# Performance work log

Hardware: AMD Instinct MI355X
Metric: run time of the kernel (lower is better)

Reference implementation:

```python
import jax, jax.numpy as jnp
import numpy as np

TOKENS, D_IN, D_OUT = 8192, 4096, 4096

def setup_inputs() -> dict:
    key = jax.random.key(0)
    k1, k2, k3 = jax.random.split(key, 3)
    x = jax.random.normal(k1, (TOKENS, D_IN), dtype=jnp.float32)
    # original init: uniform(-1, 1) on weights of shape [out, in]
    w_pos = jax.random.uniform(k2, (D_OUT, D_IN), dtype=jnp.float32, minval=-1.0, maxval=1.0)
    w_neg = jax.random.uniform(k3, (D_OUT, D_IN), dtype=jnp.float32, minval=-1.0, maxval=1.0)
    return {"x": x, "w_pos": w_pos, "w_neg": w_neg}

def _ste_binarize(w):
    # (w > 0).float() in fwd, identity grad (STE): stop_grad(bin - w) + w
    b = (w > 0).astype(w.dtype)
    return jax.lax.stop_gradient(b - w) + w

def reference(x, w_pos, w_neg):
    tern_pos = _ste_binarize(w_pos)  # [O, I]
    tern_neg = _ste_binarize(w_neg)  # [O, I]
    # y = x @ tern_pos^T - x @ tern_neg^T  (biases unused in original forward)
    y = jnp.einsum('ti,oi->to', x, tern_pos) - jnp.einsum('ti,oi->to', x, tern_neg)
    return y
```

## Files before the change

kernel.cpp:

```cpp
#include <hip/hip_runtime.h>
#include <stdint.h>


#define TOKENS 8192
#define DIN    4096
#define DOUT   4096

typedef __bf16  bf16x8  __attribute__((ext_vector_type(8)));
typedef float   floatx4 __attribute__((ext_vector_type(4)));

__device__ __forceinline__ void async_copy16(const void* g, void* l) {
  __builtin_amdgcn_global_load_lds(
      (const __attribute__((address_space(1))) void*)g,
      (__attribute__((address_space(3))) void*)l, 16, 0, 0);
}

__device__ __forceinline__ unsigned short f2bf_rne(float f) {
  union { float f; uint32_t u; } v; v.f = f;
  uint32_t u = v.u;
  u += 0x7fffu + ((u >> 16) & 1u);
  return (unsigned short)(u >> 16);
}

__device__ __forceinline__ unsigned short tern_bits(float p, float n) {
  bool bp = p > 0.0f, bn = n > 0.0f;
  return (unsigned short)(bp == bn ? 0u : (bp ? 0x3f80u : 0xbf80u));
}

__global__ __launch_bounds__(256) void prep_kernel(
    const float4* __restrict__ x, ushort4* __restrict__ xb,
    const float4* __restrict__ wp, const float4* __restrict__ wn,
    ushort4* __restrict__ t) {
  const uint32_t bid = blockIdx.x;
  if (bid < 8192u) {
    const uint32_t stride = 8192u * 256u;
    uint32_t i = bid * 256u + threadIdx.x;
#pragma unroll
    for (int it = 0; it < 4; ++it, i += stride) {
      float4 v = x[i];
      ushort4 o;
      o.x = f2bf_rne(v.x); o.y = f2bf_rne(v.y);
      o.z = f2bf_rne(v.z); o.w = f2bf_rne(v.w);
      xb[i] = o;
    }
  } else {
    const uint32_t stride = 4096u * 256u;
    uint32_t i = (bid - 8192u) * 256u + threadIdx.x;
#pragma unroll
    for (int it = 0; it < 4; ++it, i += stride) {
      float4 p = wp[i];
      float4 n = wn[i];
      ushort4 o;
      o.x = tern_bits(p.x, n.x);
      o.y = tern_bits(p.y, n.y);
      o.z = tern_bits(p.z, n.z);
      o.w = tern_bits(p.w, n.w);
      t[i] = o;
    }
  }
}


#define LDS_BUF   65536u
#define LDS_B_OFF 32768u
#define LDS_KC    16384u

__global__ __launch_bounds__(512, 2) void gemm_bt(
    const unsigned short* __restrict__ A,
    const unsigned short* __restrict__ B,
    float* __restrict__ C)
{
  __shared__ __align__(16) char lds[131072];

  const int tid   = threadIdx.x;
  const int lane  = tid & 63;
  const int wid   = tid >> 6;
  const int waveM = wid >> 2;
  const int waveN = wid & 3;

  const uint32_t flat = blockIdx.x;
  const uint32_t swz  = ((flat & 7u) << 6) | (flat >> 3);
  const uint32_t bm = (swz >> 4) * 256u;
  const uint32_t bn = (swz & 15u) * 256u;

  const uint32_t srow  = (uint32_t)(tid >> 6) * 32u + (uint32_t)((tid & 63) >> 2);
  const uint32_t slot  = (uint32_t)(tid & 3);
  const uint32_t chnk  = slot ^ ((srow >> 1) & 3u);
  const uint32_t stA   = (bm + srow) * (DIN * 2u) + chnk * 16u;
  const uint32_t stB   = (bn + srow) * (DIN * 2u) + chnk * 16u;
  const uint32_t ldsSt = (uint32_t)(tid >> 6) * 2048u + (uint32_t)(tid & 63) * 16u;
  const char* Ab = (const char*)A;
  const char* Bb = (const char*)B;

  const int mrow = lane & 15;
  const int q    = lane >> 4;
  const int xs   = (q ^ ((mrow >> 1) & 3)) * 16;
  const uint32_t ldsBase =
      (uint32_t)(uintptr_t)(__attribute__((address_space(3))) char*)lds;
  const uint32_t aFragBase = (uint32_t)waveM * 8192u + (uint32_t)mrow * 64u + (uint32_t)xs;
  const uint32_t bFragBase = LDS_B_OFF + (uint32_t)waveN * 4096u
                           + (uint32_t)mrow * 64u + (uint32_t)xs;
  const uint32_t aA0 = ldsBase + aFragBase;
  const uint32_t aA1 = aA0 + LDS_BUF;
  const uint32_t bA0 = ldsBase + bFragBase;
  const uint32_t bA1 = bA0 + LDS_BUF;

  floatx4 acc[8][4];
#pragma unroll
  for (int m = 0; m < 8; ++m)
#pragma unroll
    for (int n = 0; n < 4; ++n)
      acc[m][n] = (floatx4)0.0f;

  floatx4 a0f[4], a1f[4], b0f[4], b1f[4];

#define DSR(DST, ADDR, IMM)                                                \
  asm volatile("ds_read_b128 %0, %1 offset:%c2"                            \
               : "=v"(DST) : "v"(ADDR), "i"(IMM))

#define IA4(DST, ADDR, KC, MH) do {                                        \
    DSR(DST[0], ADDR, (KC) * 16384 + ((MH) * 4 + 0) * 1024);               \
    DSR(DST[1], ADDR, (KC) * 16384 + ((MH) * 4 + 1) * 1024);               \
    DSR(DST[2], ADDR, (KC) * 16384 + ((MH) * 4 + 2) * 1024);               \
    DSR(DST[3], ADDR, (KC) * 16384 + ((MH) * 4 + 3) * 1024);               \
  } while (0)

#define IB2(DST, N0, ADDR, KC) do {                                        \
    DSR(DST[N0],     ADDR, (KC) * 16384 + ((N0)) * 1024);                  \
    DSR(DST[N0 + 1], ADDR, (KC) * 16384 + ((N0) + 1) * 1024);              \
  } while (0)

#define STAGE_A(BUF, KH, KB) do {                                          \
    uint32_t g_ = stA + (KB) + (KH) * 64u;                                 \
    uint32_t l_ = (BUF) * LDS_BUF + (KH) * LDS_KC + ldsSt;                 \
    async_copy16(Ab + g_,           lds + l_);                             \
    async_copy16(Ab + g_ + 131072u, lds + l_ + 1024u);                     \
  } while (0)

#define STAGE_B(BUF, KH, KB) do {                                          \
    uint32_t g_ = stB + (KB) + (KH) * 64u;                                 \
    uint32_t l_ = (BUF) * LDS_BUF + LDS_B_OFF + (KH) * LDS_KC + ldsSt;     \
    async_copy16(Bb + g_,           lds + l_);                             \
    async_copy16(Bb + g_ + 131072u, lds + l_ + 1024u);                     \
  } while (0)

#define PHASE(MH, AF, BF, ISSUE_STMT, STAGE_STMT) do {                     \
    asm volatile("s_waitcnt lgkmcnt(0)" ::: "memory");                     \
    asm volatile("s_waitcnt vmcnt(8)" ::: "memory");                       \
    __builtin_amdgcn_sched_barrier(0);                                     \
    ISSUE_STMT;                                                            \
    __builtin_amdgcn_sched_barrier(0);                                     \
    __builtin_amdgcn_s_setprio(1);                                         \
    _Pragma("unroll")                                                      \
    for (int m_ = 0; m_ < 4; ++m_)                                         \
      _Pragma("unroll")                                                    \
      for (int n_ = 0; n_ < 4; ++n_)                                       \
        acc[(MH) * 4 + m_][n_] = __builtin_amdgcn_mfma_f32_16x16x32_bf16(  \
            __builtin_bit_cast(bf16x8, AF[m_]),                            \
            __builtin_bit_cast(bf16x8, BF[n_]),                            \
            acc[(MH) * 4 + m_][n_], 0, 0, 0);                              \
    __builtin_amdgcn_s_setprio(0);                                         \
    STAGE_STMT;                                                            \
    __builtin_amdgcn_s_barrier();                                          \
  } while (0)

  STAGE_B(0, 0, 0u);
  STAGE_A(0, 0, 0u);
  STAGE_B(0, 1, 0u);
  STAGE_A(0, 1, 0u);
  STAGE_B(1, 0, 128u);
  STAGE_A(1, 0, 128u);
  STAGE_B(1, 1, 128u);
  asm volatile("s_waitcnt vmcnt(8)" ::: "memory");
  __builtin_amdgcn_s_barrier();
  IB2(b0f, 0, bA0, 0); IB2(b0f, 2, bA0, 0 + 0);
  DSR(b0f[0], bA0, 0); DSR(b0f[1], bA0, 1024);
  DSR(b0f[2], bA0, 2048); DSR(b0f[3], bA0, 3072);
  IA4(a0f, aA0, 0, 0);

#pragma unroll 1
  for (int i = 0; i < 32; ++i) {
    const uint32_t kb1 = (uint32_t)(2 * i + 1) * 128u;
    const uint32_t kb2 = (uint32_t)((2 * i + 2) & 63) * 128u;
    const uint32_t kb3 = (uint32_t)((2 * i + 3) & 63) * 128u;

    PHASE(0, a0f, b0f, { IA4(a1f, aA0, 0, 1); IB2(b1f, 0, bA0, 1); },
          STAGE_A(1, 1, kb1));
    PHASE(1, a1f, b0f, { IA4(a0f, aA0, 1, 0); IB2(b1f, 2, bA0, 1); },
          STAGE_B(0, 0, kb2));
    PHASE(0, a0f, b1f, { IA4(a1f, aA0, 1, 1); IB2(b0f, 0, bA1, 0); },
          STAGE_A(0, 0, kb2));
    PHASE(1, a1f, b1f, { IA4(a0f, aA1, 0, 0); IB2(b0f, 2, bA1, 0); },
          STAGE_B(0, 1, kb2));
    PHASE(0, a0f, b0f, { IA4(a1f, aA1, 0, 1); IB2(b1f, 0, bA1, 1); },
          STAGE_A(0, 1, kb2));
    PHASE(1, a1f, b0f, { IA4(a0f, aA1, 1, 0); IB2(b1f, 2, bA1, 1); },
          STAGE_B(1, 0, kb3));
    PHASE(0, a0f, b1f, { IA4(a1f, aA1, 1, 1); IB2(b0f, 0, bA0, 0); },
          STAGE_A(1, 0, kb3));
    PHASE(1, a1f, b1f, { IA4(a0f, aA0, 0, 0); IB2(b0f, 2, bA0, 0); },
          STAGE_B(1, 1, kb3));
  }

  const int col0 = (int)bn + waveN * 64 + (lane & 15);
  const int row0 = (int)bm + waveM * 128 + (lane >> 4) * 4;
  float* Cp = C + (size_t)row0 * DOUT + col0;
#pragma unroll
  for (int m = 0; m < 8; ++m)
#pragma unroll
    for (int n = 0; n < 4; ++n)
#pragma unroll
      for (int r = 0; r < 4; ++r)
        Cp[(size_t)(m * 16 + r) * DOUT + n * 16] = acc[m][n][r];

#undef DSR
#undef IA4
#undef IB2
#undef STAGE_A
#undef STAGE_B
#undef PHASE
}

extern "C" void kernel_launch(void* const* d_in, const int* in_sizes, int n_in,
                              void* d_out, int out_size, void* d_ws, size_t ws_size,
                              hipStream_t stream) {
  const float* x  = (const float*)d_in[0];
  const float* wp = (const float*)d_in[1];
  const float* wn = (const float*)d_in[2];
  float* out = (float*)d_out;

  unsigned short* xb   = (unsigned short*)d_ws;
  unsigned short* tern = xb + (size_t)TOKENS * DIN;

  prep_kernel<<<12288, 256, 0, stream>>>(
      (const float4*)x, (ushort4*)xb,
      (const float4*)wp, (const float4*)wn, (ushort4*)tern);

  gemm_bt<<<TOKENS / 256 * (DOUT / 256), 512, 0, stream>>>(xb, tern, out);
}
```

Measured before the change: 537.1 us.

## Store LDS tiles in fragment-native order so each lane reads contiguous 16B

Changes the global-to-LDS staging mapping so each wave's 16x64-byte fragment is laid out in lane order. Each lane's ds_read_b128 then uses a plain lane*16 offset and no XOR swizzle. The vmcnt wait threshold is lowered, and a redundant set of initial B fragment reads in the prologue is removed. The global loads now cover 16 rows with 64B per row per wave instead of wider row chunks, which may hurt coalescing. The prologue still waits at vmcnt(8) while phases use vmcnt(6), which could be inconsistent.

```diff
diff --git a/kernel.cpp b/kernel.cpp
--- a/kernel.cpp
+++ b/kernel.cpp
@@ -83,27 +83,22 @@
   const uint32_t bm = (swz >> 4) * 256u;
   const uint32_t bn = (swz & 15u) * 256u;
 
-  const uint32_t srow  = (uint32_t)(tid >> 6) * 32u + (uint32_t)((tid & 63) >> 2);
-  const uint32_t slot  = (uint32_t)(tid & 3);
-  const uint32_t chnk  = slot ^ ((srow >> 1) & 3u);
-  const uint32_t stA   = (bm + srow) * (DIN * 2u) + chnk * 16u;
-  const uint32_t stB   = (bn + srow) * (DIN * 2u) + chnk * 16u;
-  const uint32_t ldsSt = (uint32_t)(tid >> 6) * 2048u + (uint32_t)(tid & 63) * 16u;
+  const uint32_t st0   = (uint32_t)(tid >> 6);
+  const uint32_t frow  = (uint32_t)(tid & 15);
+  const uint32_t fcol  = ((uint32_t)(tid >> 4) & 3u) * 16u;
+  const uint32_t stA0  = (bm + st0 * 16u + frow) * 8192u + fcol;
+  const uint32_t stB0  = (bn + st0 * 16u + frow) * 8192u + fcol;
+  const uint32_t tOff  = (uint32_t)tid * 16u;
   const char* Ab = (const char*)A;
   const char* Bb = (const char*)B;
 
-  const int mrow = lane & 15;
-  const int q    = lane >> 4;
-  const int xs   = (q ^ ((mrow >> 1) & 3)) * 16;
   const uint32_t ldsBase =
       (uint32_t)(uintptr_t)(__attribute__((address_space(3))) char*)lds;
-  const uint32_t aFragBase = (uint32_t)waveM * 8192u + (uint32_t)mrow * 64u + (uint32_t)xs;
-  const uint32_t bFragBase = LDS_B_OFF + (uint32_t)waveN * 4096u
-                           + (uint32_t)mrow * 64u + (uint32_t)xs;
-  const uint32_t aA0 = ldsBase + aFragBase;
-  const uint32_t aA1 = aA0 + LDS_BUF;
-  const uint32_t bA0 = ldsBase + bFragBase;
-  const uint32_t bA1 = bA0 + LDS_BUF;
+  const uint32_t aR0 = ldsBase + (uint32_t)waveM * 8192u + (uint32_t)lane * 16u;
+  const uint32_t aR1 = aR0 + LDS_BUF;
+  const uint32_t bR0 = ldsBase + LDS_B_OFF + (uint32_t)waveN * 4096u
+                     + (uint32_t)lane * 16u;
+  const uint32_t bR1 = bR0 + LDS_BUF;
 
   floatx4 acc[8][4];
 #pragma unroll
@@ -130,23 +125,23 @@
     DSR(DST[N0 + 1], ADDR, (KC) * 16384 + ((N0) + 1) * 1024);              \
   } while (0)
 
-#define STAGE_A(BUF, KH, KB) do {                                          \
-    uint32_t g_ = stA + (KB) + (KH) * 64u;                                 \
-    uint32_t l_ = (BUF) * LDS_BUF + (KH) * LDS_KC + ldsSt;                 \
-    async_copy16(Ab + g_,           lds + l_);                             \
-    async_copy16(Ab + g_ + 131072u, lds + l_ + 1024u);                     \
-  } while (0)
-
-#define STAGE_B(BUF, KH, KB) do {                                          \
-    uint32_t g_ = stB + (KB) + (KH) * 64u;                                 \
-    uint32_t l_ = (BUF) * LDS_BUF + LDS_B_OFF + (KH) * LDS_KC + ldsSt;     \
-    async_copy16(Bb + g_,           lds + l_);                             \
-    async_copy16(Bb + g_ + 131072u, lds + l_ + 1024u);                     \
+#define STAGE_A(BUF, KC, KB) do {                                          \
+    uint32_t g_ = stA0 + (KB) + (KC) * 64u;                                \
+    uint32_t l_ = (BUF) * LDS_BUF + (KC) * LDS_KC + tOff;                  \
+    async_copy16(Ab + g_,            lds + l_);                            \
+    async_copy16(Ab + g_ + 1048576u, lds + l_ + 8192u);                    \
+  } while (0)
+
+#define STAGE_B(BUF, KC, KB) do {                                          \
+    uint32_t g_ = stB0 + (KB) + (KC) * 64u;                                \
+    uint32_t l_ = (BUF) * LDS_BUF + LDS_B_OFF + (KC) * LDS_KC + tOff;      \
+    async_copy16(Bb + g_,            lds + l_);                            \
+    async_copy16(Bb + g_ + 1048576u, lds + l_ + 8192u);                    \
   } while (0)
 
 #define PHASE(MH, AF, BF, ISSUE_STMT, STAGE_STMT) do {                     \
     asm volatile("s_waitcnt lgkmcnt(0)" ::: "memory");                     \
-    asm volatile("s_waitcnt vmcnt(8)" ::: "memory");                       \
+    asm volatile("s_waitcnt vmcnt(6)" ::: "memory");                       \
     __builtin_amdgcn_sched_barrier(0);                                     \
     ISSUE_STMT;                                                            \
     __builtin_amdgcn_sched_barrier(0);                                     \
@@ -173,10 +168,8 @@
   STAGE_B(1, 1, 128u);
   asm volatile("s_waitcnt vmcnt(8)" ::: "memory");
   __builtin_amdgcn_s_barrier();
-  IB2(b0f, 0, bA0, 0); IB2(b0f, 2, bA0, 0 + 0);
-  DSR(b0f[0], bA0, 0); DSR(b0f[1], bA0, 1024);
-  DSR(b0f[2], bA0, 2048); DSR(b0f[3], bA0, 3072);
-  IA4(a0f, aA0, 0, 0);
+  IB2(b0f, 0, bR0, 0); IB2(b0f, 2, bR0, 0);
+  IA4(a0f, aR0, 0, 0);
 
 #pragma unroll 1
   for (int i = 0; i < 32; ++i) {
@@ -184,21 +177,21 @@
     const uint32_t kb2 = (uint32_t)((2 * i + 2) & 63) * 128u;
     const uint32_t kb3 = (uint32_t)((2 * i + 3) & 63) * 128u;
 
-    PHASE(0, a0f, b0f, { IA4(a1f, aA0, 0, 1); IB2(b1f, 0, bA0, 1); },
+    PHASE(0, a0f, b0f, { IA4(a1f, aR0, 0, 1); IB2(b1f, 0, bR0, 1); },
           STAGE_A(1, 1, kb1));
-    PHASE(1, a1f, b0f, { IA4(a0f, aA0, 1, 0); IB2(b1f, 2, bA0, 1); },
+    PHASE(1, a1f, b0f, { IA4(a0f, aR0, 1, 0); IB2(b1f, 2, bR0, 1); },
           STAGE_B(0, 0, kb2));
-    PHASE(0, a0f, b1f, { IA4(a1f, aA0, 1, 1); IB2(b0f, 0, bA1, 0); },
+    PHASE(0, a0f, b1f, { IA4(a1f, aR0, 1, 1); IB2(b0f, 0, bR1, 0); },
           STAGE_A(0, 0, kb2));
-    PHASE(1, a1f, b1f, { IA4(a0f, aA1, 0, 0); IB2(b0f, 2, bA1, 0); },
+    PHASE(1, a1f, b1f, { IA4(a0f, aR1, 0, 0); IB2(b0f, 2, bR1, 0); },
           STAGE_B(0, 1, kb2));
-    PHASE(0, a0f, b0f, { IA4(a1f, aA1, 0, 1); IB2(b1f, 0, bA1, 1); },
+    PHASE(0, a0f, b0f, { IA4(a1f, aR1, 0, 1); IB2(b1f, 0, bR1, 1); },
           STAGE_A(0, 1, kb2));
-    PHASE(1, a1f, b0f, { IA4(a0f, aA1, 1, 0); IB2(b1f, 2, bA1, 1); },
+    PHASE(1, a1f, b0f, { IA4(a0f, aR1, 1, 0); IB2(b1f, 2, bR1, 1); },
           STAGE_B(1, 0, kb3));
-    PHASE(0, a0f, b1f, { IA4(a1f, aA1, 1, 1); IB2(b0f, 0, bA0, 0); },
+    PHASE(0, a0f, b1f, { IA4(a1f, aR1, 1, 1); IB2(b0f, 0, bR0, 0); },
           STAGE_A(1, 0, kb3));
-    PHASE(1, a1f, b1f, { IA4(a0f, aA0, 0, 0); IB2(b0f, 2, bA0, 0); },
+    PHASE(1, a1f, b1f, { IA4(a0f, aR0, 0, 0); IB2(b0f, 2, bR0, 0); },
           STAGE_B(1, 1, kb3));
   }
 
```

Result: slower. 596.6 us (+11.1%).

## Fuse prep and GEMM into one persistent cooperative kernel with grid sync

Applied to the files above, without the earlier changes.

Merges the bf16 conversion and ternary weight prep with the GEMM into a single cooperative kernel of 256 blocks. Each block converts its slice with nontemporal loads, then does a grid-wide sync, then computes two 256x256 output tiles. This removes one kernel launch and the gap between the two kernels. In exchange it adds a grid barrier, and it cuts the GEMM to 256 resident blocks, which gives a tail effect when the number of CUs does not divide the work evenly. At 128KB of LDS per block, only one block fits per CU, so the launch_bounds setting of 2 blocks per CU cannot be met.

```diff
diff --git a/kernel.cpp b/kernel.cpp
--- a/kernel.cpp
+++ b/kernel.cpp
@@ -1,5 +1,8 @@
 #include <hip/hip_runtime.h>
+#include <hip/hip_cooperative_groups.h>
 #include <stdint.h>
+
+namespace cg = cooperative_groups;
 
 
 #define TOKENS 8192
@@ -8,6 +11,8 @@
 
 typedef __bf16  bf16x8  __attribute__((ext_vector_type(8)));
 typedef float   floatx4 __attribute__((ext_vector_type(4)));
+typedef float   f32x4   __attribute__((ext_vector_type(4)));
+typedef unsigned short u16x4 __attribute__((ext_vector_type(4)));
 
 __device__ __forceinline__ void async_copy16(const void* g, void* l) {
   __builtin_amdgcn_global_load_lds(
@@ -27,70 +32,61 @@
   return (unsigned short)(bp == bn ? 0u : (bp ? 0x3f80u : 0xbf80u));
 }
 
-__global__ __launch_bounds__(256) void prep_kernel(
-    const float4* __restrict__ x, ushort4* __restrict__ xb,
-    const float4* __restrict__ wp, const float4* __restrict__ wn,
-    ushort4* __restrict__ t) {
-  const uint32_t bid = blockIdx.x;
-  if (bid < 8192u) {
-    const uint32_t stride = 8192u * 256u;
-    uint32_t i = bid * 256u + threadIdx.x;
-#pragma unroll
-    for (int it = 0; it < 4; ++it, i += stride) {
-      float4 v = x[i];
-      ushort4 o;
+
+#define LDS_BUF   65536u
+#define LDS_B_OFF 32768u
+#define LDS_KC    16384u
+
+__global__ __launch_bounds__(512, 2) void fused_kernel(
+    const float* __restrict__ x,
+    const float* __restrict__ wp,
+    const float* __restrict__ wn,
+    unsigned short* __restrict__ xb,
+    unsigned short* __restrict__ tern,
+    float* __restrict__ C)
+{
+  __shared__ __align__(16) char lds[131072];
+
+  const int tid = threadIdx.x;
+  const uint32_t b = blockIdx.x;
+
+  {
+    const f32x4* xf = (const f32x4*)x;
+    u16x4* xo = (u16x4*)xb;
+    uint32_t i = b * 32768u + (uint32_t)tid;
+#pragma unroll 4
+    for (int j = 0; j < 64; ++j, i += 512u) {
+      f32x4 v = __builtin_nontemporal_load(&xf[i]);
+      u16x4 o;
       o.x = f2bf_rne(v.x); o.y = f2bf_rne(v.y);
       o.z = f2bf_rne(v.z); o.w = f2bf_rne(v.w);
-      xb[i] = o;
+      xo[i] = o;
     }
-  } else {
-    const uint32_t stride = 4096u * 256u;
-    uint32_t i = (bid - 8192u) * 256u + threadIdx.x;
-#pragma unroll
-    for (int it = 0; it < 4; ++it, i += stride) {
-      float4 p = wp[i];
-      float4 n = wn[i];
-      ushort4 o;
+    const f32x4* wpf = (const f32x4*)wp;
+    const f32x4* wnf = (const f32x4*)wn;
+    u16x4* to = (u16x4*)tern;
+    uint32_t k = b * 16384u + (uint32_t)tid;
+#pragma unroll 4
+    for (int j = 0; j < 32; ++j, k += 512u) {
+      f32x4 p = __builtin_nontemporal_load(&wpf[k]);
+      f32x4 n = __builtin_nontemporal_load(&wnf[k]);
+      u16x4 o;
       o.x = tern_bits(p.x, n.x);
       o.y = tern_bits(p.y, n.y);
       o.z = tern_bits(p.z, n.z);
       o.w = tern_bits(p.w, n.w);
-      t[i] = o;
+      to[k] = o;
     }
   }
-}
-
-
-#define LDS_BUF   65536u
-#define LDS_B_OFF 32768u
-#define LDS_KC    16384u
-
-__global__ __launch_bounds__(512, 2) void gemm_bt(
-    const unsigned short* __restrict__ A,
-    const unsigned short* __restrict__ B,
-    float* __restrict__ C)
-{
-  __shared__ __align__(16) char lds[131072];
-
-  const int tid   = threadIdx.x;
+
+  asm volatile("s_waitcnt vmcnt(0) lgkmcnt(0)" ::: "memory");
+  cg::this_grid().sync();
+  __builtin_amdgcn_sched_barrier(0);
+
   const int lane  = tid & 63;
   const int wid   = tid >> 6;
   const int waveM = wid >> 2;
   const int waveN = wid & 3;
-
-  const uint32_t flat = blockIdx.x;
-  const uint32_t swz  = ((flat & 7u) << 6) | (flat >> 3);
-  const uint32_t bm = (swz >> 4) * 256u;
-  const uint32_t bn = (swz & 15u) * 256u;
-
-  const uint32_t srow  = (uint32_t)(tid >> 6) * 32u + (uint32_t)((tid & 63) >> 2);
-  const uint32_t slot  = (uint32_t)(tid & 3);
-  const uint32_t chnk  = slot ^ ((srow >> 1) & 3u);
-  const uint32_t stA   = (bm + srow) * (DIN * 2u) + chnk * 16u;
-  const uint32_t stB   = (bn + srow) * (DIN * 2u) + chnk * 16u;
-  const uint32_t ldsSt = (uint32_t)(tid >> 6) * 2048u + (uint32_t)(tid & 63) * 16u;
-  const char* Ab = (const char*)A;
-  const char* Bb = (const char*)B;
 
   const int mrow = lane & 15;
   const int q    = lane >> 4;
@@ -105,14 +101,16 @@
   const uint32_t bA0 = ldsBase + bFragBase;
   const uint32_t bA1 = bA0 + LDS_BUF;
 
+  const uint32_t srow  = (uint32_t)wid * 32u + (uint32_t)(lane >> 2);
+  const uint32_t slot  = (uint32_t)(tid & 3);
+  const uint32_t chnk  = slot ^ ((srow >> 1) & 3u);
+  const uint32_t ldsSt = (uint32_t)(tid >> 6) * 2048u
+                       + (uint32_t)(tid & 63) * 16u;
+  const char* Ab = (const char*)xb;
+  const char* Bb = (const char*)tern;
+
+  floatx4 a0f[4], a1f[4], b0f[4], b1f[4];
   floatx4 acc[8][4];
-#pragma unroll
-  for (int m = 0; m < 8; ++m)
-#pragma unroll
-    for (int n = 0; n < 4; ++n)
-      acc[m][n] = (floatx4)0.0f;
-
-  floatx4 a0f[4], a1f[4], b0f[4], b1f[4];
 
 #define DSR(DST, ADDR, IMM)                                                \
   asm volatile("ds_read_b128 %0, %1 offset:%c2"                            \
@@ -164,54 +162,72 @@
     __builtin_amdgcn_s_barrier();                                          \
   } while (0)
 
-  STAGE_B(0, 0, 0u);
-  STAGE_A(0, 0, 0u);
-  STAGE_B(0, 1, 0u);
-  STAGE_A(0, 1, 0u);
-  STAGE_B(1, 0, 128u);
-  STAGE_A(1, 0, 128u);
-  STAGE_B(1, 1, 128u);
-  asm volatile("s_waitcnt vmcnt(8)" ::: "memory");
-  __builtin_amdgcn_s_barrier();
-  IB2(b0f, 0, bA0, 0); IB2(b0f, 2, bA0, 0 + 0);
-  DSR(b0f[0], bA0, 0); DSR(b0f[1], bA0, 1024);
-  DSR(b0f[2], bA0, 2048); DSR(b0f[3], bA0, 3072);
-  IA4(a0f, aA0, 0, 0);
-
 #pragma unroll 1
-  for (int i = 0; i < 32; ++i) {
-    const uint32_t kb1 = (uint32_t)(2 * i + 1) * 128u;
-    const uint32_t kb2 = (uint32_t)((2 * i + 2) & 63) * 128u;
-    const uint32_t kb3 = (uint32_t)((2 * i + 3) & 63) * 128u;
-
-    PHASE(0, a0f, b0f, { IA4(a1f, aA0, 0, 1); IB2(b1f, 0, bA0, 1); },
-          STAGE_A(1, 1, kb1));
-    PHASE(1, a1f, b0f, { IA4(a0f, aA0, 1, 0); IB2(b1f, 2, bA0, 1); },
-          STAGE_B(0, 0, kb2));
-    PHASE(0, a0f, b1f, { IA4(a1f, aA0, 1, 1); IB2(b0f, 0, bA1, 0); },
-          STAGE_A(0, 0, kb2));
-    PHASE(1, a1f, b1f, { IA4(a0f, aA1, 0, 0); IB2(b0f, 2, bA1, 0); },
-          STAGE_B(0, 1, kb2));
-    PHASE(0, a0f, b0f, { IA4(a1f, aA1, 0, 1); IB2(b1f, 0, bA1, 1); },
-          STAGE_A(0, 1, kb2));
-    PHASE(1, a1f, b0f, { IA4(a0f, aA1, 1, 0); IB2(b1f, 2, bA1, 1); },
-          STAGE_B(1, 0, kb3));
-    PHASE(0, a0f, b1f, { IA4(a1f, aA1, 1, 1); IB2(b0f, 0, bA0, 0); },
-          STAGE_A(1, 0, kb3));
-    PHASE(1, a1f, b1f, { IA4(a0f, aA0, 0, 0); IB2(b0f, 2, bA0, 0); },
-          STAGE_B(1, 1, kb3));
+  for (int t = 0; t < 2; ++t) {
+    const uint32_t flat = b + (uint32_t)t * 256u;
+    const uint32_t swz  = ((flat & 7u) << 6) | (flat >> 3);
+    const uint32_t bm = (swz >> 4) * 256u;
+    const uint32_t bn = (swz & 15u) * 256u;
+    const uint32_t stA = (bm + srow) * (DIN * 2u) + chnk * 16u;
+    const uint32_t stB = (bn + srow) * (DIN * 2u) + chnk * 16u;
+
+#pragma unroll
+    for (int m = 0; m < 8; ++m)
+#pragma unroll
+      for (int n = 0; n < 4; ++n)
+        acc[m][n] = (floatx4)0.0f;
+
+    asm volatile("s_waitcnt lgkmcnt(0)" ::: "memory");
+    asm volatile("s_waitcnt vmcnt(0)" ::: "memory");
+    __builtin_amdgcn_s_barrier();
+
+    STAGE_B(0, 0, 0u);
+    STAGE_A(0, 0, 0u);
+    STAGE_B(0, 1, 0u);
+    STAGE_A(0, 1, 0u);
+    STAGE_B(1, 0, 128u);
+    STAGE_A(1, 0, 128u);
+    STAGE_B(1, 1, 128u);
+    asm volatile("s_waitcnt vmcnt(8)" ::: "memory");
+    __builtin_amdgcn_s_barrier();
+    IB2(b0f, 0, bA0, 0); IB2(b0f, 2, bA0, 0);
+    IA4(a0f, aA0, 0, 0);
+
+#pragma unroll 1
+    for (int i = 0; i < 32; ++i) {
+      const uint32_t kb1 = (uint32_t)(2 * i + 1) * 128u;
+      const uint32_t kb2 = (uint32_t)((2 * i + 2) & 63) * 128u;
+      const uint32_t kb3 = (uint32_t)((2 * i + 3) & 63) * 128u;
+
+      PHASE(0, a0f, b0f, { IA4(a1f, aA0, 0, 1); IB2(b1f, 0, bA0, 1); },
+            STAGE_A(1, 1, kb1));
+      PHASE(1, a1f, b0f, { IA4(a0f, aA0, 1, 0); IB2(b1f, 2, bA0, 1); },
+            STAGE_B(0, 0, kb2));
+      PHASE(0, a0f, b1f, { IA4(a1f, aA0, 1, 1); IB2(b0f, 0, bA1, 0); },
+            STAGE_A(0, 0, kb2));
+      PHASE(1, a1f, b1f, { IA4(a0f, aA1, 0, 0); IB2(b0f, 2, bA1, 0); },
+            STAGE_B(0, 1, kb2));
+      PHASE(0, a0f, b0f, { IA4(a1f, aA1, 0, 1); IB2(b1f, 0, bA1, 1); },
+            STAGE_A(0, 1, kb2));
+      PHASE(1, a1f, b0f, { IA4(a0f, aA1, 1, 0); IB2(b1f, 2, bA1, 1); },
+            STAGE_B(1, 0, kb3));
+      PHASE(0, a0f, b1f, { IA4(a1f, aA1, 1, 1); IB2(b0f, 0, bA0, 0); },
+            STAGE_A(1, 0, kb3));
+      PHASE(1, a1f, b1f, { IA4(a0f, aA0, 0, 0); IB2(b0f, 2, bA0, 0); },
+            STAGE_B(1, 1, kb3));
+    }
+
+    const int col0 = (int)bn + waveN * 64 + (lane & 15);
+    const int row0 = (int)bm + waveM * 128 + (lane >> 4) * 4;
+    float* Cp = C + (size_t)row0 * DOUT + col0;
+#pragma unroll
+    for (int m = 0; m < 8; ++m)
+#pragma unroll
+      for (int n = 0; n < 4; ++n)
+#pragma unroll
+        for (int r = 0; r < 4; ++r)
+          Cp[(size_t)(m * 16 + r) * DOUT + n * 16] = acc[m][n][r];
   }
-
-  const int col0 = (int)bn + waveN * 64 + (lane & 15);
-  const int row0 = (int)bm + waveM * 128 + (lane >> 4) * 4;
-  float* Cp = C + (size_t)row0 * DOUT + col0;
-#pragma unroll
-  for (int m = 0; m < 8; ++m)
-#pragma unroll
-    for (int n = 0; n < 4; ++n)
-#pragma unroll
-      for (int r = 0; r < 4; ++r)
-        Cp[(size_t)(m * 16 + r) * DOUT + n * 16] = acc[m][n][r];
 
 #undef DSR
 #undef IA4
@@ -232,9 +248,10 @@
   unsigned short* xb   = (unsigned short*)d_ws;
   unsigned short* tern = xb + (size_t)TOKENS * DIN;
 
-  prep_kernel<<<12288, 256, 0, stream>>>(
-      (const float4*)x, (ushort4*)xb,
-      (const float4*)wp, (const float4*)wn, (ushort4*)tern);
-
-  gemm_bt<<<TOKENS / 256 * (DOUT / 256), 512, 0, stream>>>(xb, tern, out);
-}
+  void* args[6] = {
+      (void*)&x, (void*)&wp, (void*)&wn,
+      (void*)&xb, (void*)&tern, (void*)&out,
+  };
+  (void)hipLaunchCooperativeKernel((const void*)fused_kernel,
+                                   dim3(256), dim3(512), args, 0, stream);
+}
```

New measurement: 528.5 us. About the same (-1.6%).
